# Kernel optimization log

Measured on AMD Instinct MI355X. Metric: run time of the kernel, lower is better.

The kernel has to match this reference:

```python
import jax, jax.numpy as jnp
import numpy as np

N = 20000          # num nodes
E_EDGES = 160000   # num edges
D = 128            # input feature dim
H = 128            # hidden dim
C = 128            # num_classes (expert output dim)
NE = 4             # num_experts
COEF = 0.01        # load-balancing loss coefficient


def setup_inputs() -> dict:
    key = jax.random.key(0)
    ks = jax.random.split(key, 8)
    x = jax.random.normal(ks[0], (N, D), jnp.float32)
    edge_index = jax.random.randint(ks[1], (2, E_EDGES), 0, N)
    x_agg = jax.random.normal(ks[2], (N, D), jnp.float32)
    # gate params (w_gate is zeros-init in source; use small randn so gating is exercised)
    w_gate = jax.random.normal(ks[3], (D, NE), jnp.float32) * 0.1
    gate_threshold = jax.random.normal(ks[4], (NE,), jnp.float32) * 0.1
    experts_mask = jnp.ones((NE,), jnp.float32)
    # per-expert 2-layer GCN weights (vectorized over expert dim)
    W1 = jax.random.normal(ks[5], (NE, D, H), jnp.float32) * (1.0 / np.sqrt(D))
    b1 = jnp.zeros((NE, H), jnp.float32)
    W2 = jax.random.normal(ks[6], (NE, H, C), jnp.float32) * (1.0 / np.sqrt(H))
    b2 = jnp.zeros((NE, C), jnp.float32)
    return {"x": x, "edge_index": edge_index, "x_agg": x_agg,
            "w_gate": w_gate, "gate_threshold": gate_threshold,
            "experts_mask": experts_mask, "W1": W1, "b1": b1, "W2": W2, "b2": b2}


def _gcn_norm(edge_index):
    src, dst = edge_index[0], edge_index[1]
    deg = jax.ops.segment_sum(jnp.ones((src.shape[0],), jnp.float32), dst, num_segments=N)
    deg = jnp.maximum(deg, 1.0)
    norm = jax.lax.rsqrt(deg[src] * deg[dst])  # symmetric GCN normalization per edge
    return src, dst, norm


def _agg(h, src, dst, norm):
    # h: [N, F] -> normalized neighbor sum: [N, F]
    return jax.ops.segment_sum(h[src] * norm[:, None], dst, num_segments=N)


def _ste_sign(s):
    # SAGMMGateBackward: sign in forward, identity in backward (straight-through)
    return s + jax.lax.stop_gradient(jnp.sign(s) - s)


def reference(x, edge_index, x_agg, w_gate, gate_threshold, experts_mask, W1, b1, W2, b2):
    src, dst, norm = _gcn_norm(edge_index)

    # --- noisy_top_any gating (eval path: no noise), add_sigmoid=True ---
    clean_logits = x_agg @ w_gate                       # [N, NE]
    gate_scores = jax.nn.sigmoid(clean_logits)          # [N, NE]
    # sign-based straight-through gate vs learned threshold, masked by experts_mask
    gates = jax.nn.relu(_ste_sign(gate_scores - gate_threshold[None, :]))
    gates = gates * experts_mask[None, :]               # [N, NE], binary in forward

    # --- experts: 4 two-layer GCNs, vectorized over the expert dim ---
    agg_x = _agg(x, src, dst, norm)                     # shared first aggregation [N, D]
    h = jax.nn.relu(jnp.einsum('nd,edh->enh', agg_x, W1) + b1[:, None, :])   # [NE, N, H]
    agg_h = jax.vmap(lambda hh: _agg(hh, src, dst, norm))(h)                 # [NE, N, H]
    expert_out = jnp.einsum('enh,ehc->enc', agg_h, W2) + b2[:, None, :]      # [NE, N, C]

    # --- combine expert outputs with gates ---
    output = jnp.einsum('ne,enc->nc', gates, expert_out)                     # [N, C]

    # --- cv_squared load-balancing loss on per-expert importance ---
    importance = gates.sum(axis=0)                                           # [NE]
    load_loss = COEF * (jnp.var(importance) / (jnp.mean(importance) ** 2 + 1e-10))
    return output, load_loss
```

## Files before the change

kernel.cpp:

```cpp
#include <hip/hip_runtime.h>
#include <cstdint>
#include <cstddef>

#define NNODES 20000
#define NEDGES 160000
#define DFEAT  128
#define NEXP   4

typedef unsigned short u16;
typedef __attribute__((ext_vector_type(8))) short short8v;
typedef __attribute__((ext_vector_type(4))) float float4v;

static __device__ __forceinline__ u16 f2bf(float f) {
    union { float f; unsigned int i; } v; v.f = f;
    unsigned int r = (v.i + 0x7FFFu + ((v.i >> 16) & 1u)) >> 16;
    return (u16)r;
}
static __device__ __forceinline__ unsigned pack2(float a, float b) {
    return ((unsigned)f2bf(b) << 16) | f2bf(a);
}
static __device__ __forceinline__ float lo2f(unsigned int u) { return __uint_as_float(u << 16); }
static __device__ __forceinline__ float hi2f(unsigned int u) { return __uint_as_float(u & 0xFFFF0000u); }

static __device__ __forceinline__ void acc8(float w, uint4 v, float* a) {
    a[0] += w * lo2f(v.x); a[1] += w * hi2f(v.x);
    a[2] += w * lo2f(v.y); a[3] += w * hi2f(v.y);
    a[4] += w * lo2f(v.z); a[5] += w * hi2f(v.z);
    a[6] += w * lo2f(v.w); a[7] += w * hi2f(v.w);
}


__global__ void k_pre(const int* __restrict__ ei, const float* __restrict__ x,
                      const float* __restrict__ W1, const float* __restrict__ W2,
                      const float* __restrict__ x_agg, const float* __restrict__ w_gate,
                      const float* __restrict__ thr, const float* __restrict__ mask,
                      float* __restrict__ deg, u16* __restrict__ W1t, u16* __restrict__ W2t,
                      float* __restrict__ gates, float* __restrict__ importance,
                      u16* __restrict__ xbf) {
    int b = blockIdx.x;
    if (b < 625) {
        int e = b * 256 + threadIdx.x;
        if (e < NEDGES) atomicAdd(&deg[ei[NEDGES + e]], 1.0f);
        return;
    }
    if (b < 753) {
        __shared__ u16 tile[32][33];
        int tb = b - 625;
        int arr = tb >> 6;
        int t6 = tb & 63;
        int e  = t6 >> 4;
        int kt = (t6 >> 2) & 3;
        int ct = t6 & 3;
        const float* W = arr ? W2 : W1;
        u16* Wt = arr ? W2t : W1t;
        int ty = threadIdx.x >> 5, tx = threadIdx.x & 31;
#pragma unroll
        for (int r = 0; r < 4; ++r) {
            int k = kt * 32 + ty + r * 8;
            int c = ct * 32 + tx;
            tile[ty + r * 8][tx] = f2bf(W[(size_t)e * 16384 + (size_t)k * 128 + c]);
        }
        __syncthreads();
#pragma unroll
        for (int r = 0; r < 4; ++r) {
            int c = ct * 32 + ty + r * 8;
            int k = kt * 32 + tx;
            Wt[(size_t)e * 16384 + (size_t)c * 128 + k] = tile[tx][ty + r * 8];
        }
        return;
    }
    if (b < 832) {
        int n = (b - 753) * 256 + threadIdx.x;
        float4 lg = make_float4(0.f, 0.f, 0.f, 0.f);
        if (n < NNODES) {
            const float4* xr = (const float4*)(x_agg + (size_t)n * DFEAT);
            const float4* wg = (const float4*)w_gate;
            for (int k4 = 0; k4 < 32; ++k4) {
                float4 xv = xr[k4];
                float4 w0 = wg[4 * k4 + 0], w1 = wg[4 * k4 + 1];
                float4 w2 = wg[4 * k4 + 2], w3 = wg[4 * k4 + 3];
                lg.x += xv.x * w0.x + xv.y * w1.x + xv.z * w2.x + xv.w * w3.x;
                lg.y += xv.x * w0.y + xv.y * w1.y + xv.z * w2.y + xv.w * w3.y;
                lg.z += xv.x * w0.z + xv.y * w1.z + xv.z * w2.z + xv.w * w3.z;
                lg.w += xv.x * w0.w + xv.y * w1.w + xv.z * w2.w + xv.w * w3.w;
            }
        }
        float g[4];
        float lv[4] = {lg.x, lg.y, lg.z, lg.w};
        for (int e = 0; e < 4; ++e) {
            float sgm = 1.0f / (1.0f + expf(-lv[e]));
            g[e] = (sgm - thr[e] > 0.0f) ? mask[e] : 0.0f;
            if (n >= NNODES) g[e] = 0.0f;
        }
        if (n < NNODES) ((float4*)gates)[n] = make_float4(g[0], g[1], g[2], g[3]);
        int lane = threadIdx.x & 63;
        for (int e = 0; e < 4; ++e) {
            float v = g[e];
            for (int off = 32; off >= 1; off >>= 1) v += __shfl_down(v, off);
            if (lane == 0) atomicAdd(&importance[e], v);
        }
        return;
    }
    int t8 = (b - 832) * 256 + threadIdx.x;
    const float4* xr = (const float4*)x + (size_t)t8 * 2;
    float4 v0 = xr[0], v1 = xr[1];
    uint4 o;
    o.x = pack2(v0.x, v0.y); o.y = pack2(v0.z, v0.w);
    o.z = pack2(v1.x, v1.y); o.w = pack2(v1.z, v1.w);
    ((uint4*)xbf)[t8] = o;
}

__global__ void k_scan(const float* __restrict__ deg, int* __restrict__ rowstart) {
    __shared__ int part[1024];
    int t = threadIdx.x;
    const int PER = 20;
    int base = t * PER;
    int s = 0;
    for (int i = 0; i < PER; ++i) {
        int n = base + i;
        if (n < NNODES) s += (int)deg[n];
    }
    part[t] = s;
    __syncthreads();
    for (int off = 1; off < 1024; off <<= 1) {
        int v = (t >= off) ? part[t - off] : 0;
        __syncthreads();
        part[t] += v;
        __syncthreads();
    }
    int run = part[t] - s;
    for (int i = 0; i < PER; ++i) {
        int n = base + i;
        if (n < NNODES) {
            rowstart[n] = run;
            run += (int)deg[n];
        }
    }
    if (t == 1023) rowstart[NNODES] = part[1023];
}

__global__ void k_fill(const int* __restrict__ ei, const float* __restrict__ deg,
                       const int* __restrict__ rowstart, int* __restrict__ cursor,
                       int* __restrict__ csrc, float* __restrict__ cnrm) {
    int e = blockIdx.x * 256 + threadIdx.x;
    if (e >= NEDGES) return;
    int s = ei[e], d = ei[NEDGES + e];
    int pos = atomicAdd(&cursor[d], 1);
    int slot = rowstart[d] + pos;
    csrc[slot] = s;
    float ds = fmaxf(deg[s], 1.0f), dd = fmaxf(deg[d], 1.0f);
    cnrm[slot] = 1.0f / sqrtf(ds * dd);
}

__launch_bounds__(320)
__global__ void k_ag1(const u16* __restrict__ xbf, const int* __restrict__ rowstart,
                      const int* __restrict__ csrc, const float* __restrict__ cnrm,
                      const u16* __restrict__ W1t, const float* __restrict__ b1,
                      u16* __restrict__ h) {
    __shared__ uint4 As[80 * 17];
    int t = threadIdx.x;
    int nbase = blockIdx.x * 80;

    for (int it = t; it < 1280; it += 320) {
        int nl = it >> 4, l8 = it & 15;
        int node = nbase + nl;
        int r0 = rowstart[node], r1 = rowstart[node + 1];
        float a[8] = {0.f, 0.f, 0.f, 0.f, 0.f, 0.f, 0.f, 0.f};
        int j = r0;
        for (; j + 4 <= r1; j += 4) {
            int s0 = csrc[j], s1 = csrc[j + 1], s2 = csrc[j + 2], s3 = csrc[j + 3];
            float w0 = cnrm[j], w1 = cnrm[j + 1], w2 = cnrm[j + 2], w3 = cnrm[j + 3];
            uint4 v0 = ((const uint4*)(xbf + (size_t)s0 * DFEAT))[l8];
            uint4 v1 = ((const uint4*)(xbf + (size_t)s1 * DFEAT))[l8];
            uint4 v2 = ((const uint4*)(xbf + (size_t)s2 * DFEAT))[l8];
            uint4 v3 = ((const uint4*)(xbf + (size_t)s3 * DFEAT))[l8];
            acc8(w0, v0, a); acc8(w1, v1, a); acc8(w2, v2, a); acc8(w3, v3, a);
        }
        for (; j < r1; ++j) {
            uint4 v = ((const uint4*)(xbf + (size_t)csrc[j] * DFEAT))[l8];
            acc8(cnrm[j], v, a);
        }
        uint4 o;
        o.x = pack2(a[0], a[1]); o.y = pack2(a[2], a[3]);
        o.z = pack2(a[4], a[5]); o.w = pack2(a[6], a[7]);
        As[nl * 17 + l8] = o;
    }
    __syncthreads();

    int w = t >> 6, l = t & 63;
    int lr = l & 15, kg = l >> 4;
    const short8v* As8 = (const short8v*)As;
    short8v a[4];
#pragma unroll
    for (int kk = 0; kk < 4; ++kk) a[kk] = As8[(w * 16 + lr) * 17 + kk * 4 + kg];

#pragma unroll
    for (int e = 0; e < NEXP; ++e) {
        const short8v* B8 = (const short8v*)(W1t + (size_t)e * 16384);
        u16* hb = h + (size_t)e * NNODES * DFEAT;
#pragma unroll
        for (int c = 0; c < 8; ++c) {
            float4v acc = {0.f, 0.f, 0.f, 0.f};
#pragma unroll
            for (int kk = 0; kk < 4; ++kk) {
                short8v bfr = B8[(c * 16 + lr) * 16 + kk * 4 + kg];
                acc = __builtin_amdgcn_mfma_f32_16x16x32_bf16(a[kk], bfr, acc, 0, 0, 0);
            }
            float bv = b1[e * DFEAT + c * 16 + lr];
#pragma unroll
            for (int i = 0; i < 4; ++i) {
                int node = nbase + w * 16 + kg * 4 + i;
                float vv = fmaxf(acc[i] + bv, 0.f);
                hb[(size_t)node * DFEAT + c * 16 + lr] = f2bf(vv);
            }
        }
    }
}

__launch_bounds__(320)
__global__ void k_ag2(const u16* __restrict__ h, const int* __restrict__ rowstart,
                      const int* __restrict__ csrc, const float* __restrict__ cnrm,
                      const u16* __restrict__ W2t, const float* __restrict__ b2,
                      const float* __restrict__ gates, const float* __restrict__ importance,
                      float* __restrict__ out) {
    if (blockIdx.x == 0 && threadIdx.x == 0) {
        float v0 = importance[0], v1 = importance[1], v2 = importance[2], v3 = importance[3];
        float mean = 0.25f * (v0 + v1 + v2 + v3);
        float d0 = v0 - mean, d1 = v1 - mean, d2 = v2 - mean, d3 = v3 - mean;
        float var = 0.25f * (d0 * d0 + d1 * d1 + d2 * d2 + d3 * d3);
        out[(size_t)NNODES * DFEAT] = 0.01f * var / (mean * mean + 1e-10f);
    }
    __shared__ uint4 As[80 * 17];
    int t = threadIdx.x;
    int nbase = blockIdx.x * 80;
    int w = t >> 6, l = t & 63;
    int lr = l & 15, kg = l >> 4;
    const short8v* As8 = (const short8v*)As;

    float4v acc[8];
#pragma unroll
    for (int c = 0; c < 8; ++c) acc[c] = (float4v){0.f, 0.f, 0.f, 0.f};

    float gw[4];

    for (int e = 0; e < NEXP; ++e) {
        __syncthreads();
        const u16* hb = h + (size_t)e * NNODES * DFEAT;
        for (int it = t; it < 1280; it += 320) {
            int nl = it >> 4, l8 = it & 15;
            int node = nbase + nl;
            uint4 o = make_uint4(0u, 0u, 0u, 0u);
            if (gates[(size_t)node * 4 + e] != 0.0f) {
                int r0 = rowstart[node], r1 = rowstart[node + 1];
                float a[8] = {0.f, 0.f, 0.f, 0.f, 0.f, 0.f, 0.f, 0.f};
                int j = r0;
                for (; j + 4 <= r1; j += 4) {
                    int s0 = csrc[j], s1 = csrc[j + 1], s2 = csrc[j + 2], s3 = csrc[j + 3];
                    float w0 = cnrm[j], w1 = cnrm[j + 1], w2 = cnrm[j + 2], w3 = cnrm[j + 3];
                    uint4 v0 = ((const uint4*)(hb + (size_t)s0 * DFEAT))[l8];
                    uint4 v1 = ((const uint4*)(hb + (size_t)s1 * DFEAT))[l8];
                    uint4 v2 = ((const uint4*)(hb + (size_t)s2 * DFEAT))[l8];
                    uint4 v3 = ((const uint4*)(hb + (size_t)s3 * DFEAT))[l8];
                    acc8(w0, v0, a); acc8(w1, v1, a); acc8(w2, v2, a); acc8(w3, v3, a);
                }
                for (; j < r1; ++j) {
                    uint4 v = ((const uint4*)(hb + (size_t)csrc[j] * DFEAT))[l8];
                    acc8(cnrm[j], v, a);
                }
                o.x = pack2(a[0], a[1]); o.y = pack2(a[2], a[3]);
                o.z = pack2(a[4], a[5]); o.w = pack2(a[6], a[7]);
            }
            As[nl * 17 + l8] = o;
        }
        __syncthreads();

        short8v a[4];
#pragma unroll
        for (int kk = 0; kk < 4; ++kk) a[kk] = As8[(w * 16 + lr) * 17 + kk * 4 + kg];
#pragma unroll
        for (int i = 0; i < 4; ++i)
            gw[i] = gates[(size_t)(nbase + w * 16 + kg * 4 + i) * 4 + e];
        const short8v* B8 = (const short8v*)(W2t + (size_t)e * 16384);
#pragma unroll
        for (int c = 0; c < 8; ++c) {
            float4v tv = {0.f, 0.f, 0.f, 0.f};
#pragma unroll
            for (int kk = 0; kk < 4; ++kk) {
                short8v bfr = B8[(c * 16 + lr) * 16 + kk * 4 + kg];
                tv = __builtin_amdgcn_mfma_f32_16x16x32_bf16(a[kk], bfr, tv, 0, 0, 0);
            }
            float bv = b2[e * DFEAT + c * 16 + lr];
#pragma unroll
            for (int i = 0; i < 4; ++i) acc[c][i] += gw[i] * (tv[i] + bv);
        }
    }

#pragma unroll
    for (int c = 0; c < 8; ++c)
#pragma unroll
        for (int i = 0; i < 4; ++i) {
            int node = nbase + w * 16 + kg * 4 + i;
            out[(size_t)node * DFEAT + c * 16 + lr] = acc[c][i];
        }
}

extern "C" void kernel_launch(void* const* d_in, const int* in_sizes, int n_in,
                              void* d_out, int out_size, void* d_ws, size_t ws_size,
                              hipStream_t stream) {
    const float* x      = (const float*)d_in[0];
    const int*   ei     = (const int*)d_in[1];
    const float* x_agg  = (const float*)d_in[2];
    const float* w_gate = (const float*)d_in[3];
    const float* thr    = (const float*)d_in[4];
    const float* mask   = (const float*)d_in[5];
    const float* W1     = (const float*)d_in[6];
    const float* b1     = (const float*)d_in[7];
    const float* W2     = (const float*)d_in[8];
    const float* b2     = (const float*)d_in[9];
    float* out = (float*)d_out;
    float* ws  = (float*)d_ws;

    float* deg        = ws;
    int*   cursor     = (int*)(ws + 20000);
    float* importance = ws + 40000;
    int*   rowstart   = (int*)(ws + 40960);
    int*   csrc       = (int*)(ws + 61440);
    float* cnrm       = ws + 221440;
    float* gates      = ws + 381440;
    u16*   W1t        = (u16*)(ws + 461440);
    u16*   W2t        = (u16*)(ws + 494208);
    u16*   xbf        = (u16*)(ws + 526976);
    u16*   h          = (u16*)(ws + 1806976);

    hipMemsetAsync(d_ws, 0, 40008 * sizeof(float), stream);

    k_pre<<<2082, 256, 0, stream>>>(ei, x, W1, W2, x_agg, w_gate, thr, mask,
                                    deg, W1t, W2t, gates, importance, xbf);
    k_scan<<<1, 1024, 0, stream>>>(deg, rowstart);
    k_fill<<<(NEDGES + 255) / 256, 256, 0, stream>>>(ei, deg, rowstart, cursor, csrc, cnrm);
    k_ag1<<<250, 320, 0, stream>>>(xbf, rowstart, csrc, cnrm, W1t, b1, h);
    k_ag2<<<250, 320, 0, stream>>>(h, rowstart, csrc, cnrm, W2t, b2, gates, importance, out);
}
```

Before: 284.1 us.

## Shrink aggregation tiles to 32 nodes and gather all experts before MFMA

Both aggregation kernels now handle 32 nodes per block with 256 threads, launching 625 blocks instead of 250. That spreads the work over more CUs on the MI355X, which has 256. Each wave now covers a 16-row by 64-column quarter of the output tile instead of a full 16x128 row strip. In k_ag2, the gathers for all four experts are issued in one pass into a larger shared buffer with a single barrier, instead of four serialized gather/sync/MFMA phases. This exposes more memory-level parallelism, at the cost of more LDS per block and some repeated B-fragment loads across blocks.

```diff
diff --git a/kernel.cpp b/kernel.cpp
--- a/kernel.cpp
+++ b/kernel.cpp
@@ -152,16 +152,16 @@
     cnrm[slot] = 1.0f / sqrtf(ds * dd);
 }
 
-__launch_bounds__(320)
+__launch_bounds__(256)
 __global__ void k_ag1(const u16* __restrict__ xbf, const int* __restrict__ rowstart,
                       const int* __restrict__ csrc, const float* __restrict__ cnrm,
                       const u16* __restrict__ W1t, const float* __restrict__ b1,
                       u16* __restrict__ h) {
-    __shared__ uint4 As[80 * 17];
+    __shared__ uint4 As[32 * 17];
     int t = threadIdx.x;
-    int nbase = blockIdx.x * 80;
-
-    for (int it = t; it < 1280; it += 320) {
+    int nbase = blockIdx.x * 32;
+
+    for (int it = t; it < 512; it += 256) {
         int nl = it >> 4, l8 = it & 15;
         int node = nbase + nl;
         int r0 = rowstart[node], r1 = rowstart[node + 1];
@@ -188,36 +188,37 @@
     __syncthreads();
 
     int w = t >> 6, l = t & 63;
+    int rh = w & 1, ch = w >> 1;
     int lr = l & 15, kg = l >> 4;
     const short8v* As8 = (const short8v*)As;
     short8v a[4];
 #pragma unroll
-    for (int kk = 0; kk < 4; ++kk) a[kk] = As8[(w * 16 + lr) * 17 + kk * 4 + kg];
+    for (int kk = 0; kk < 4; ++kk) a[kk] = As8[(rh * 16 + lr) * 17 + kk * 4 + kg];
 
 #pragma unroll
     for (int e = 0; e < NEXP; ++e) {
         const short8v* B8 = (const short8v*)(W1t + (size_t)e * 16384);
         u16* hb = h + (size_t)e * NNODES * DFEAT;
 #pragma unroll
-        for (int c = 0; c < 8; ++c) {
+        for (int c = 0; c < 4; ++c) {
             float4v acc = {0.f, 0.f, 0.f, 0.f};
 #pragma unroll
             for (int kk = 0; kk < 4; ++kk) {
-                short8v bfr = B8[(c * 16 + lr) * 16 + kk * 4 + kg];
+                short8v bfr = B8[((ch * 4 + c) * 16 + lr) * 16 + kk * 4 + kg];
                 acc = __builtin_amdgcn_mfma_f32_16x16x32_bf16(a[kk], bfr, acc, 0, 0, 0);
             }
-            float bv = b1[e * DFEAT + c * 16 + lr];
+            float bv = b1[e * DFEAT + (ch * 4 + c) * 16 + lr];
 #pragma unroll
             for (int i = 0; i < 4; ++i) {
-                int node = nbase + w * 16 + kg * 4 + i;
+                int node = nbase + rh * 16 + kg * 4 + i;
                 float vv = fmaxf(acc[i] + bv, 0.f);
-                hb[(size_t)node * DFEAT + c * 16 + lr] = f2bf(vv);
-            }
-        }
-    }
-}
-
-__launch_bounds__(320)
+                hb[(size_t)node * DFEAT + (ch * 4 + c) * 16 + lr] = f2bf(vv);
+            }
+        }
+    }
+}
+
+__launch_bounds__(256)
 __global__ void k_ag2(const u16* __restrict__ h, const int* __restrict__ rowstart,
                       const int* __restrict__ csrc, const float* __restrict__ cnrm,
                       const u16* __restrict__ W2t, const float* __restrict__ b2,
@@ -230,77 +231,81 @@
         float var = 0.25f * (d0 * d0 + d1 * d1 + d2 * d2 + d3 * d3);
         out[(size_t)NNODES * DFEAT] = 0.01f * var / (mean * mean + 1e-10f);
     }
-    __shared__ uint4 As[80 * 17];
+    __shared__ uint4 As[4 * 32 * 17];
     int t = threadIdx.x;
-    int nbase = blockIdx.x * 80;
+    int nbase = blockIdx.x * 32;
+
+    for (int it = t; it < 2048; it += 256) {
+        int e = it >> 9;
+        int rem = it & 511;
+        int nl = rem >> 4, l8 = rem & 15;
+        int node = nbase + nl;
+        uint4 o = make_uint4(0u, 0u, 0u, 0u);
+        if (gates[(size_t)node * 4 + e] != 0.0f) {
+            const u16* hb = h + (size_t)e * NNODES * DFEAT;
+            int r0 = rowstart[node], r1 = rowstart[node + 1];
+            float a[8] = {0.f, 0.f, 0.f, 0.f, 0.f, 0.f, 0.f, 0.f};
+            int j = r0;
+            for (; j + 4 <= r1; j += 4) {
+                int s0 = csrc[j], s1 = csrc[j + 1], s2 = csrc[j + 2], s3 = csrc[j + 3];
+                float w0 = cnrm[j], w1 = cnrm[j + 1], w2 = cnrm[j + 2], w3 = cnrm[j + 3];
+                uint4 v0 = ((const uint4*)(hb + (size_t)s0 * DFEAT))[l8];
+                uint4 v1 = ((const uint4*)(hb + (size_t)s1 * DFEAT))[l8];
+                uint4 v2 = ((const uint4*)(hb + (size_t)s2 * DFEAT))[l8];
+                uint4 v3 = ((const uint4*)(hb + (size_t)s3 * DFEAT))[l8];
+                acc8(w0, v0, a); acc8(w1, v1, a); acc8(w2, v2, a); acc8(w3, v3, a);
+            }
+            for (; j < r1; ++j) {
+                uint4 v = ((const uint4*)(hb + (size_t)csrc[j] * DFEAT))[l8];
+                acc8(cnrm[j], v, a);
+            }
+            o.x = pack2(a[0], a[1]); o.y = pack2(a[2], a[3]);
+            o.z = pack2(a[4], a[5]); o.w = pack2(a[6], a[7]);
+        }
+        As[(e * 32 + nl) * 17 + l8] = o;
+    }
+    __syncthreads();
+
     int w = t >> 6, l = t & 63;
+    int rh = w & 1, ch = w >> 1;
     int lr = l & 15, kg = l >> 4;
     const short8v* As8 = (const short8v*)As;
 
-    float4v acc[8];
-#pragma unroll
-    for (int c = 0; c < 8; ++c) acc[c] = (float4v){0.f, 0.f, 0.f, 0.f};
-
-    float gw[4];
-
+    float4v acc[4];
+#pragma unroll
+    for (int c = 0; c < 4; ++c) acc[c] = (float4v){0.f, 0.f, 0.f, 0.f};
+
+#pragma unroll
     for (int e = 0; e < NEXP; ++e) {
-        __syncthreads();
-        const u16* hb = h + (size_t)e * NNODES * DFEAT;
-        for (int it = t; it < 1280; it += 320) {
-            int nl = it >> 4, l8 = it & 15;
-            int node = nbase + nl;
-            uint4 o = make_uint4(0u, 0u, 0u, 0u);
-            if (gates[(size_t)node * 4 + e] != 0.0f) {
-                int r0 = rowstart[node], r1 = rowstart[node + 1];
-                float a[8] = {0.f, 0.f, 0.f, 0.f, 0.f, 0.f, 0.f, 0.f};
-                int j = r0;
-                for (; j + 4 <= r1; j += 4) {
-                    int s0 = csrc[j], s1 = csrc[j + 1], s2 = csrc[j + 2], s3 = csrc[j + 3];
-                    float w0 = cnrm[j], w1 = cnrm[j + 1], w2 = cnrm[j + 2], w3 = cnrm[j + 3];
-                    uint4 v0 = ((const uint4*)(hb + (size_t)s0 * DFEAT))[l8];
-                    uint4 v1 = ((const uint4*)(hb + (size_t)s1 * DFEAT))[l8];
-                    uint4 v2 = ((const uint4*)(hb + (size_t)s2 * DFEAT))[l8];
-                    uint4 v3 = ((const uint4*)(hb + (size_t)s3 * DFEAT))[l8];
-                    acc8(w0, v0, a); acc8(w1, v1, a); acc8(w2, v2, a); acc8(w3, v3, a);
-                }
-                for (; j < r1; ++j) {
-                    uint4 v = ((const uint4*)(hb + (size_t)csrc[j] * DFEAT))[l8];
-                    acc8(cnrm[j], v, a);
-                }
-                o.x = pack2(a[0], a[1]); o.y = pack2(a[2], a[3]);
-                o.z = pack2(a[4], a[5]); o.w = pack2(a[6], a[7]);
-            }
-            As[nl * 17 + l8] = o;
-        }
-        __syncthreads();
-
         short8v a[4];
 #pragma unroll
-        for (int kk = 0; kk < 4; ++kk) a[kk] = As8[(w * 16 + lr) * 17 + kk * 4 + kg];
+        for (int kk = 0; kk < 4; ++kk)
+            a[kk] = As8[((e * 32) + rh * 16 + lr) * 17 + kk * 4 + kg];
+        float gw[4];
 #pragma unroll
         for (int i = 0; i < 4; ++i)
-            gw[i] = gates[(size_t)(nbase + w * 16 + kg * 4 + i) * 4 + e];
+            gw[i] = gates[(size_t)(nbase + rh * 16 + kg * 4 + i) * 4 + e];
         const short8v* B8 = (const short8v*)(W2t + (size_t)e * 16384);
 #pragma unroll
-        for (int c = 0; c < 8; ++c) {
+        for (int c = 0; c < 4; ++c) {
             float4v tv = {0.f, 0.f, 0.f, 0.f};
 #pragma unroll
             for (int kk = 0; kk < 4; ++kk) {
-                short8v bfr = B8[(c * 16 + lr) * 16 + kk * 4 + kg];
+                short8v bfr = B8[((ch * 4 + c) * 16 + lr) * 16 + kk * 4 + kg];
                 tv = __builtin_amdgcn_mfma_f32_16x16x32_bf16(a[kk], bfr, tv, 0, 0, 0);
             }
-            float bv = b2[e * DFEAT + c * 16 + lr];
+            float bv = b2[e * DFEAT + (ch * 4 + c) * 16 + lr];
 #pragma unroll
             for (int i = 0; i < 4; ++i) acc[c][i] += gw[i] * (tv[i] + bv);
         }
     }
 
 #pragma unroll
-    for (int c = 0; c < 8; ++c)
+    for (int c = 0; c < 4; ++c)
 #pragma unroll
         for (int i = 0; i < 4; ++i) {
-            int node = nbase + w * 16 + kg * 4 + i;
-            out[(size_t)node * DFEAT + c * 16 + lr] = acc[c][i];
+            int node = nbase + rh * 16 + kg * 4 + i;
+            out[(size_t)node * DFEAT + (ch * 4 + c) * 16 + lr] = acc[c][i];
         }
 }
 
@@ -338,6 +343,6 @@
                                     deg, W1t, W2t, gates, importance, xbf);
     k_scan<<<1, 1024, 0, stream>>>(deg, rowstart);
     k_fill<<<(NEDGES + 255) / 256, 256, 0, stream>>>(ei, deg, rowstart, cursor, csrc, cnrm);
-    k_ag1<<<250, 320, 0, stream>>>(xbf, rowstart, csrc, cnrm, W1t, b1, h);
-    k_ag2<<<250, 320, 0, stream>>>(h, rowstart, csrc, cnrm, W2t, b2, gates, importance, out);
-}
+    k_ag1<<<625, 256, 0, stream>>>(xbf, rowstart, csrc, cnrm, W1t, b1, h);
+    k_ag2<<<625, 256, 0, stream>>>(h, rowstart, csrc, cnrm, W2t, b2, gates, importance, out);
+}
```

New measurement: 248.6 us. 12.5% less time.
